# Kernel optimization log

Measured on AMD Instinct MI355X. Metric: run time of the kernel, lower is better.

## Reference

```python
import jax, jax.numpy as jnp
import numpy as np

N_HEAD = 4
D_MODEL = 256
D_K = D_MODEL // N_HEAD  # 64
B, S = 8, 2048


def _xavier(key, shape):
    fan_in, fan_out = shape[-1], shape[-2]
    a = jnp.sqrt(6.0 / (fan_in + fan_out))
    return jax.random.uniform(key, shape, jnp.float32, -a, a)


def setup_inputs() -> dict:
    key = jax.random.key(0)
    ks = jax.random.split(key, 8)
    q = jax.random.normal(ks[0], (B, S, D_MODEL), jnp.float32)
    k = jax.random.normal(ks[1], (B, S, D_MODEL), jnp.float32)
    v = jax.random.normal(ks[2], (B, S, D_MODEL), jnp.float32)
    # stacked per-head projections: [H, d_k, d_model] (torch Linear weight layout)
    Wq = _xavier(ks[3], (N_HEAD, D_K, D_MODEL))
    Wk = _xavier(ks[4], (N_HEAD, D_K, D_MODEL))
    bq = jnp.zeros((N_HEAD, D_K), jnp.float32)
    bk = jnp.zeros((N_HEAD, D_K), jnp.float32)
    Wv = _xavier(ks[5], (D_K, D_MODEL))
    bv = jnp.zeros((D_K,), jnp.float32)
    Wh = _xavier(ks[6], (D_MODEL, D_K))  # w_h: Linear(d_v, d_model, bias=False)
    return {"q": q, "k": k, "v": v, "Wq": Wq, "bq": bq, "Wk": Wk,
            "bk": bk, "Wv": Wv, "bv": bv, "Wh": Wh}


def reference(q, k, v, Wq, bq, Wk, bk, Wv, bv, Wh):
    # shared value projection: [B,S,d_k]
    vs = jnp.einsum('bsd,ed->bse', v, Wv) + bv
    # per-head q/k projections, batched over heads: [B,H,S,d_k]
    qs = jnp.einsum('bsd,hed->bhse', q, Wq) + bq[None, :, None, :]
    ks_ = jnp.einsum('bsd,hed->bhse', k, Wk) + bk[None, :, None, :]
    scale = jnp.sqrt(jnp.asarray(D_K, qs.dtype))
    scores = jnp.einsum('bhqe,bhke->bhqk', qs, ks_) / scale
    attn = jax.nn.softmax(scores, axis=-1)  # [B,H,Sq,Sk]
    heads = jnp.einsum('bhqk,bke->bhqe', attn, vs)  # shared V
    out = jnp.mean(heads, axis=1)  # head-averaged: [B,S,d_k]
    out = jnp.einsum('bse,de->bsd', out, Wh)  # [B,S,d_model]
    attn_out = jnp.transpose(attn, (0, 2, 1, 3))  # stack(dim=2): [B,Sq,H,Sk]
    return out, attn_out
```

## Files before the change

### kernel.cpp

```cpp
#include <hip/hip_runtime.h>

typedef _Float16 half8 __attribute__((ext_vector_type(8)));
typedef _Float16 half2v __attribute__((ext_vector_type(2)));
typedef float f32x4 __attribute__((ext_vector_type(4)));

static constexpr int Bc  = 8;
static constexpr int Sc  = 2048;
static constexpr int Hc  = 4;
static constexpr int DKc = 64;
static constexpr int DMc = 256;
static constexpr int TR  = 8;
static constexpr int QT  = 64;
static constexpr int KT  = 128;
static constexpr int NKT = Sc / KT;

__global__ __launch_bounds__(256) void proj_kernel(
    const float* __restrict__ q, const float* __restrict__ k, const float* __restrict__ v,
    const float* __restrict__ Wq, const float* __restrict__ bq,
    const float* __restrict__ Wk, const float* __restrict__ bk,
    const float* __restrict__ Wv, const float* __restrict__ bv,
    _Float16* __restrict__ qs_h, _Float16* __restrict__ ks_h,
    _Float16* __restrict__ vsT) {
  const int bs0 = blockIdx.x * TR;
  const int b   = bs0 >> 11;
  const int s0  = bs0 & (Sc - 1);
  const int tid = threadIdx.x;
  __shared__ float qrow[TR][DMc], krow[TR][DMc], vrow[TR][DMc];
  {
    const float4* qg = (const float4*)(q + (size_t)bs0 * DMc);
    const float4* kg = (const float4*)(k + (size_t)bs0 * DMc);
    const float4* vg = (const float4*)(v + (size_t)bs0 * DMc);
    float4* qls = (float4*)&qrow[0][0];
    float4* kls = (float4*)&krow[0][0];
    float4* vls = (float4*)&vrow[0][0];
#pragma unroll
    for (int i = 0; i < 2; ++i) {
      qls[tid + i * 256] = qg[tid + i * 256];
      kls[tid + i * 256] = kg[tid + i * 256];
      vls[tid + i * 256] = vg[tid + i * 256];
    }
  }
  __syncthreads();
  const int h = tid >> 6, e = tid & 63;
  const float4* wq4 = (const float4*)(Wq + (size_t)(h * DKc + e) * DMc);
  const float4* wk4 = (const float4*)(Wk + (size_t)(h * DKc + e) * DMc);
  const float4* wv4 = (const float4*)(Wv + (size_t)e * DMc);
  const int rv = h * 2;
  float accq[TR], acck[TR];
  float accv0 = 0.f, accv1 = 0.f;
#pragma unroll
  for (int r = 0; r < TR; ++r) { accq[r] = 0.f; acck[r] = 0.f; }
#pragma unroll 4
  for (int i = 0; i < DMc / 4; ++i) {
    const float4 wa = wq4[i], wc = wk4[i], wv = wv4[i];
#pragma unroll
    for (int r = 0; r < TR; ++r) {
      const float4 a = ((const float4*)qrow[r])[i];
      accq[r] += a.x * wa.x + a.y * wa.y + a.z * wa.z + a.w * wa.w;
      const float4 c = ((const float4*)krow[r])[i];
      acck[r] += c.x * wc.x + c.y * wc.y + c.z * wc.z + c.w * wc.w;
    }
    const float4 a0 = ((const float4*)vrow[rv])[i];
    const float4 a1 = ((const float4*)vrow[rv + 1])[i];
    accv0 += a0.x * wv.x + a0.y * wv.y + a0.z * wv.z + a0.w * wv.w;
    accv1 += a1.x * wv.x + a1.y * wv.y + a1.z * wv.z + a1.w * wv.w;
  }
  const float bqv = bq[h * DKc + e], bkv = bk[h * DKc + e];
#pragma unroll
  for (int r = 0; r < TR; ++r) {
    const size_t row = (size_t)(b * Hc + h) * Sc + s0 + r;
    qs_h[row * DKc + e] = (_Float16)((accq[r] + bqv) * 0.125f);
    ks_h[row * DKc + e] = (_Float16)(acck[r] + bkv);
  }
  const float bvv = bv[e];
  half2v hv;
  hv[0] = (_Float16)(accv0 + bvv);
  hv[1] = (_Float16)(accv1 + bvv);
  *(half2v*)&vsT[(size_t)(b * DKc + e) * Sc + s0 + rv] = hv;
}

__global__ __launch_bounds__(256) void attn_kernel(
    const _Float16* __restrict__ qs_h, const _Float16* __restrict__ ks_h,
    const _Float16* __restrict__ vsT, float* __restrict__ attn,
    float* __restrict__ heads) {
  const int q0  = blockIdx.x * QT;
  const int h   = blockIdx.y;
  const int b   = blockIdx.z;
  const int tid = threadIdx.x;
  const int wid = tid >> 6, lane = tid & 63;
  const int lq  = lane & 15, lg = lane >> 4;
  const int qb  = q0 + wid * 16;

  __shared__ _Float16 Pl[4][16][136];

  const size_t bh = (size_t)(b * Hc + h) * Sc;
  const half8 aq0 = *(const half8*)&qs_h[(bh + qb + lq) * DKc + lg * 8];
  const half8 aq1 = *(const half8*)&qs_h[(bh + qb + lq) * DKc + 32 + lg * 8];

  float m[4], l[4];
#pragma unroll
  for (int j = 0; j < 4; ++j) { m[j] = -1e30f; l[j] = 0.f; }

  for (int kt = 0; kt < NKT; ++kt) {
    const int k0 = kt * KT;
    f32x4 lgt[8];
#pragma unroll
    for (int nt = 0; nt < 8; ++nt) {
      f32x4 c = {0.f, 0.f, 0.f, 0.f};
      const _Float16* kp = &ks_h[(bh + k0 + nt * 16 + lq) * DKc + lg * 8];
      c = __builtin_amdgcn_mfma_f32_16x16x32_f16(aq0, *(const half8*)kp, c, 0, 0, 0);
      c = __builtin_amdgcn_mfma_f32_16x16x32_f16(aq1, *(const half8*)(kp + 32), c, 0, 0, 0);
      lgt[nt] = c;
    }
#pragma unroll
    for (int j = 0; j < 4; ++j) {
      float tm = lgt[0][j];
#pragma unroll
      for (int nt = 1; nt < 8; ++nt) tm = fmaxf(tm, lgt[nt][j]);
#pragma unroll
      for (int mk = 1; mk < 16; mk <<= 1) tm = fmaxf(tm, __shfl_xor(tm, mk, 64));
      const float nm = fmaxf(m[j], tm);
      float ts = 0.f;
#pragma unroll
      for (int nt = 0; nt < 8; ++nt) ts += __expf(lgt[nt][j] - nm);
#pragma unroll
      for (int mk = 1; mk < 16; mk <<= 1) ts += __shfl_xor(ts, mk, 64);
      l[j] = l[j] * __expf(m[j] - nm) + ts;
      m[j] = nm;
    }
  }
  float inv[4];
#pragma unroll
  for (int j = 0; j < 4; ++j) inv[j] = 1.f / l[j];

  f32x4 oacc[4];
#pragma unroll
  for (int et = 0; et < 4; ++et) oacc[et] = (f32x4){0.f, 0.f, 0.f, 0.f};

  for (int kt = 0; kt < NKT; ++kt) {
    const int k0 = kt * KT;
#pragma unroll
    for (int nt = 0; nt < 8; ++nt) {
      f32x4 c = {0.f, 0.f, 0.f, 0.f};
      const _Float16* kp = &ks_h[(bh + k0 + nt * 16 + lq) * DKc + lg * 8];
      c = __builtin_amdgcn_mfma_f32_16x16x32_f16(aq0, *(const half8*)kp, c, 0, 0, 0);
      c = __builtin_amdgcn_mfma_f32_16x16x32_f16(aq1, *(const half8*)(kp + 32), c, 0, 0, 0);
#pragma unroll
      for (int j = 0; j < 4; ++j) {
        const float p = __expf(c[j] - m[j]) * inv[j];
        attn[((size_t)(b * Sc + qb + lg * 4 + j) * Hc + h) * Sc + k0 + nt * 16 + lq] = p;
        Pl[wid][lg * 4 + j][nt * 16 + lq] = (_Float16)p;
      }
    }
    asm volatile("s_waitcnt lgkmcnt(0)" ::: "memory");
#pragma unroll
    for (int ch = 0; ch < 4; ++ch) {
      const half8 ap = *(const half8*)&Pl[wid][lq][ch * 32 + lg * 8];
#pragma unroll
      for (int et = 0; et < 4; ++et) {
        const half8 bv = *(const half8*)&vsT[((size_t)b * DKc + et * 16 + lq) * Sc + k0 + ch * 32 + lg * 8];
        oacc[et] = __builtin_amdgcn_mfma_f32_16x16x32_f16(ap, bv, oacc[et], 0, 0, 0);
      }
    }
    asm volatile("" ::: "memory");
  }
#pragma unroll
  for (int et = 0; et < 4; ++et)
#pragma unroll
    for (int j = 0; j < 4; ++j)
      heads[(bh + qb + lg * 4 + j) * DKc + et * 16 + lq] = oacc[et][j];
}

__global__ __launch_bounds__(256) void out_kernel(
    const float* __restrict__ heads, const float* __restrict__ Wh,
    float* __restrict__ out) {
  const int bs0 = blockIdx.x * TR;
  const int b   = bs0 >> 11;
  const int s0  = bs0 & (Sc - 1);
  const int tid = threadIdx.x;
  __shared__ float havg[TR][DKc];
  for (int t = tid; t < TR * DKc; t += 256) {
    const int r = t >> 6, ee = t & 63;
    float a = 0.f;
#pragma unroll
    for (int hh = 0; hh < Hc; ++hh)
      a += heads[((size_t)(b * Hc + hh) * Sc + s0 + r) * DKc + ee];
    havg[r][ee] = a * 0.25f;
  }
  __syncthreads();
  const float4* wh4 = (const float4*)(Wh + (size_t)tid * DKc);
  float acc[TR];
#pragma unroll
  for (int r = 0; r < TR; ++r) acc[r] = 0.f;
#pragma unroll
  for (int i = 0; i < DKc / 4; ++i) {
    const float4 w = wh4[i];
#pragma unroll
    for (int r = 0; r < TR; ++r) {
      const float4 a = ((const float4*)havg[r])[i];
      acc[r] += a.x * w.x + a.y * w.y + a.z * w.z + a.w * w.w;
    }
  }
#pragma unroll
  for (int r = 0; r < TR; ++r)
    out[(size_t)(bs0 + r) * DMc + tid] = acc[r];
}

extern "C" void kernel_launch(void* const* d_in, const int* in_sizes, int n_in,
                              void* d_out, int out_size, void* d_ws, size_t ws_size,
                              hipStream_t stream) {
  const float* q  = (const float*)d_in[0];
  const float* k  = (const float*)d_in[1];
  const float* v  = (const float*)d_in[2];
  const float* Wq = (const float*)d_in[3];
  const float* bq = (const float*)d_in[4];
  const float* Wk = (const float*)d_in[5];
  const float* bk = (const float*)d_in[6];
  const float* Wv = (const float*)d_in[7];
  const float* bv = (const float*)d_in[8];
  const float* Wh = (const float*)d_in[9];

  float* out  = (float*)d_out;
  float* attn = out + (size_t)Bc * Sc * DMc;

  const size_t NQ = (size_t)Bc * Hc * Sc * DKc;
  _Float16* qs_h = (_Float16*)d_ws;
  _Float16* ks_h = qs_h + NQ;
  _Float16* vsT  = ks_h + NQ;
  float* heads   = (float*)(vsT + (size_t)Bc * DKc * Sc);

  proj_kernel<<<Bc * Sc / TR, 256, 0, stream>>>(q, k, v, Wq, bq, Wk, bk, Wv, bv,
                                                qs_h, ks_h, vsT);
  attn_kernel<<<dim3(Sc / QT, Hc, Bc), 256, 0, stream>>>(qs_h, ks_h, vsT, attn, heads);
  out_kernel<<<Bc * Sc / TR, 256, 0, stream>>>(heads, Wh, out);
}
```

Before: 1.153 ms.

## Defer softmax cross-lane reduction, fold normalization into exponent, prefetch V tiles

```diff
diff --git a/kernel.cpp b/kernel.cpp
--- a/kernel.cpp
+++ b/kernel.cpp
@@ -79,7 +79,7 @@
   *(half2v*)&vsT[(size_t)(b * DKc + e) * Sc + s0 + rv] = hv;
 }
 
-__global__ __launch_bounds__(256) void attn_kernel(
+__global__ __launch_bounds__(256, 4) void attn_kernel(
     const _Float16* __restrict__ qs_h, const _Float16* __restrict__ ks_h,
     const _Float16* __restrict__ vsT, float* __restrict__ attn,
     float* __restrict__ heads) {
@@ -101,6 +101,7 @@
 #pragma unroll
   for (int j = 0; j < 4; ++j) { m[j] = -1e30f; l[j] = 0.f; }
 
+#pragma unroll 2
   for (int kt = 0; kt < NKT; ++kt) {
     const int k0 = kt * KT;
     f32x4 lgt[8];
@@ -117,28 +118,42 @@
       float tm = lgt[0][j];
 #pragma unroll
       for (int nt = 1; nt < 8; ++nt) tm = fmaxf(tm, lgt[nt][j]);
-#pragma unroll
-      for (int mk = 1; mk < 16; mk <<= 1) tm = fmaxf(tm, __shfl_xor(tm, mk, 64));
       const float nm = fmaxf(m[j], tm);
       float ts = 0.f;
 #pragma unroll
       for (int nt = 0; nt < 8; ++nt) ts += __expf(lgt[nt][j] - nm);
-#pragma unroll
-      for (int mk = 1; mk < 16; mk <<= 1) ts += __shfl_xor(ts, mk, 64);
       l[j] = l[j] * __expf(m[j] - nm) + ts;
       m[j] = nm;
     }
   }
-  float inv[4];
-#pragma unroll
-  for (int j = 0; j < 4; ++j) inv[j] = 1.f / l[j];
+  float mm[4];
+#pragma unroll
+  for (int j = 0; j < 4; ++j) {
+#pragma unroll
+    for (int mk = 1; mk < 16; mk <<= 1) {
+      const float om = __shfl_xor(m[j], mk, 64);
+      const float ol = __shfl_xor(l[j], mk, 64);
+      const float nm = fmaxf(m[j], om);
+      l[j] = l[j] * __expf(m[j] - nm) + ol * __expf(om - nm);
+      m[j] = nm;
+    }
+    mm[j] = m[j] + __logf(l[j]);
+  }
 
   f32x4 oacc[4];
 #pragma unroll
   for (int et = 0; et < 4; ++et) oacc[et] = (f32x4){0.f, 0.f, 0.f, 0.f};
 
+  const _Float16* vb = vsT + (size_t)b * DKc * Sc;
   for (int kt = 0; kt < NKT; ++kt) {
     const int k0 = kt * KT;
+    half8 bva[2][4];
+#pragma unroll
+    for (int ch = 0; ch < 2; ++ch)
+#pragma unroll
+      for (int et = 0; et < 4; ++et)
+        bva[ch][et] = *(const half8*)&vb[(size_t)(et * 16 + lq) * Sc + k0 + ch * 32 + lg * 8];
+
 #pragma unroll
     for (int nt = 0; nt < 8; ++nt) {
       f32x4 c = {0.f, 0.f, 0.f, 0.f};
@@ -147,22 +162,30 @@
       c = __builtin_amdgcn_mfma_f32_16x16x32_f16(aq1, *(const half8*)(kp + 32), c, 0, 0, 0);
 #pragma unroll
       for (int j = 0; j < 4; ++j) {
-        const float p = __expf(c[j] - m[j]) * inv[j];
+        const float p = __expf(c[j] - mm[j]);
         attn[((size_t)(b * Sc + qb + lg * 4 + j) * Hc + h) * Sc + k0 + nt * 16 + lq] = p;
         Pl[wid][lg * 4 + j][nt * 16 + lq] = (_Float16)p;
       }
     }
     asm volatile("s_waitcnt lgkmcnt(0)" ::: "memory");
-#pragma unroll
-    for (int ch = 0; ch < 4; ++ch) {
+    __builtin_amdgcn_s_setprio(1);
+#pragma unroll
+    for (int ch = 0; ch < 2; ++ch) {
       const half8 ap = *(const half8*)&Pl[wid][lq][ch * 32 + lg * 8];
 #pragma unroll
+      for (int et = 0; et < 4; ++et)
+        oacc[et] = __builtin_amdgcn_mfma_f32_16x16x32_f16(ap, bva[ch][et], oacc[et], 0, 0, 0);
+    }
+#pragma unroll
+    for (int ch = 2; ch < 4; ++ch) {
+      const half8 ap = *(const half8*)&Pl[wid][lq][ch * 32 + lg * 8];
+#pragma unroll
       for (int et = 0; et < 4; ++et) {
-        const half8 bv = *(const half8*)&vsT[((size_t)b * DKc + et * 16 + lq) * Sc + k0 + ch * 32 + lg * 8];
+        const half8 bv = *(const half8*)&vb[(size_t)(et * 16 + lq) * Sc + k0 + ch * 32 + lg * 8];
         oacc[et] = __builtin_amdgcn_mfma_f32_16x16x32_f16(ap, bv, oacc[et], 0, 0, 0);
       }
     }
-    asm volatile("" ::: "memory");
+    __builtin_amdgcn_s_setprio(0);
   }
 #pragma unroll
   for (int et = 0; et < 4; ++et)
```

Measured after the change: 1.080 ms. 6.3% less time.
